# Kernel optimization log

Hardware: AMD Instinct MI355X
Metric: run time of the kernel (lower is better)

## Reference

```python
import jax, jax.numpy as jnp
import numpy as np

HIDDEN = 4096
N_HEADS = 32
N_KV_HEADS = 8
HEAD_DIM = 128
ROPE_THETA = 10000.0


def setup_inputs() -> dict:
    key = jax.random.key(0)
    ks = jax.random.split(key, 5)
    B, S = 1, 2048
    scale = 0.02
    return {
        "hidden_states": jax.random.normal(ks[0], (B, S, HIDDEN), dtype=jnp.float32),
        "q_w": jax.random.normal(ks[1], (N_HEADS * HEAD_DIM, HIDDEN), dtype=jnp.float32) * scale,
        "k_w": jax.random.normal(ks[2], (N_KV_HEADS * HEAD_DIM, HIDDEN), dtype=jnp.float32) * scale,
        "v_w": jax.random.normal(ks[3], (N_KV_HEADS * HEAD_DIM, HIDDEN), dtype=jnp.float32) * scale,
        "o_w": jax.random.normal(ks[4], (HIDDEN, N_HEADS * HEAD_DIM), dtype=jnp.float32) * scale,
        "position_ids": jnp.arange(S, dtype=jnp.int64 if jax.config.jax_enable_x64 else jnp.int32)[None, :],
    }


def _rotate_half(x):
    h = x.shape[-1] // 2
    return jnp.concatenate((-x[..., h:], x[..., :h]), axis=-1)


def _rope_cos_sin(position_ids, dtype):
    # default rope: inv_freq = theta^(-arange(0,hd,2)/hd), attention_scaling = 1
    inv_freq = 1.0 / (ROPE_THETA ** (jnp.arange(0, HEAD_DIM, 2, dtype=jnp.float32) / HEAD_DIM))
    freqs = position_ids.astype(jnp.float32)[:, :, None] * inv_freq[None, None, :]  # [B,S,hd/2]
    emb = jnp.concatenate((freqs, freqs), axis=-1)  # [B,S,hd]
    return jnp.cos(emb).astype(dtype), jnp.sin(emb).astype(dtype)


def reference(hidden_states, q_w, k_w, v_w, o_w, position_ids):
    B, S, _ = hidden_states.shape
    n_rep = N_HEADS // N_KV_HEADS

    q = (hidden_states @ q_w.T).reshape(B, S, N_HEADS, HEAD_DIM).transpose(0, 2, 1, 3)
    k = (hidden_states @ k_w.T).reshape(B, S, N_KV_HEADS, HEAD_DIM).transpose(0, 2, 1, 3)
    v = (hidden_states @ v_w.T).reshape(B, S, N_KV_HEADS, HEAD_DIM).transpose(0, 2, 1, 3)

    cos, sin = _rope_cos_sin(position_ids, hidden_states.dtype)
    cos = cos[:, None, :, :]  # unsqueeze head dim
    sin = sin[:, None, :, :]
    q = q * cos + _rotate_half(q) * sin
    k = k * cos + _rotate_half(k) * sin

    # repeat_kv (GQA)
    k = jnp.repeat(k, n_rep, axis=1)  # [B,H,S,hd]
    v = jnp.repeat(v, n_rep, axis=1)

    scale = HEAD_DIM ** -0.5
    scores = jnp.einsum("bhqd,bhkd->bhqk", q, k) * scale  # [B,H,S,S]
    causal = jnp.tril(jnp.ones((S, S), dtype=bool))
    scores = jnp.where(causal[None, None, :, :], scores, jnp.finfo(scores.dtype).min)
    probs = jax.nn.softmax(scores, axis=-1)
    attn = jnp.einsum("bhqk,bhkd->bhqd", probs, v)  # [B,H,S,hd]

    attn = attn.transpose(0, 2, 1, 3).reshape(B, S, N_HEADS * HEAD_DIM)
    return attn @ o_w.T
```

## Files before the change

kernel.cpp:

```cpp
#include <hip/hip_runtime.h>
#include <hip/hip_bf16.h>

#define NH   32
#define NKV  8
#define HD   128
#define SL   2048
#define HID  4096
#define KVW  1024
#define QKVN 6144

typedef __attribute__((ext_vector_type(8))) short short8;
typedef __attribute__((ext_vector_type(4))) float f32x4;

static __device__ __forceinline__ unsigned short f2bf(float f){
  union { float f; unsigned int i; } v; v.f = f;
  unsigned int r = v.i + 0x7FFFu + ((v.i >> 16) & 1u);
  return (unsigned short)(r >> 16);
}
static __device__ __forceinline__ float bf2f(unsigned short u){
  union { unsigned int i; float f; } v; v.i = ((unsigned int)u) << 16; return v.f;
}
static __device__ __forceinline__ unsigned int pack2(float lo, float hi){
  return (unsigned int)f2bf(lo) | ((unsigned int)f2bf(hi) << 16);
}

static __device__ __forceinline__ void gload_lds16(const void* g, void* l){
  __builtin_amdgcn_global_load_lds(
      (const __attribute__((address_space(1))) void*)g,
      (__attribute__((address_space(3))) void*)l,
      16, 0, 0);
}

__global__ void cast_f32_bf16(const float* __restrict__ src, uint4* __restrict__ dst, int n8){
  int stride = gridDim.x * blockDim.x;
  for (int i = blockIdx.x * blockDim.x + threadIdx.x; i < n8; i += stride){
    float4 a = ((const float4*)src)[2*i + 0];
    float4 b = ((const float4*)src)[2*i + 1];
    uint4 o;
    o.x = pack2(a.x, a.y); o.y = pack2(a.z, a.w);
    o.z = pack2(b.x, b.y); o.w = pack2(b.z, b.w);
    dst[i] = o;
  }
}

__global__ void rope_table_kernel(const int* __restrict__ pos, float2* __restrict__ tab){
  int i = blockIdx.x * blockDim.x + threadIdx.x;
  if (i >= SL * 64) return;
  int s = i >> 6, f = i & 63;
  float inv = expf(-((float)(2 * f) / 128.0f) * 9.210340371976184f);
  float ang = (float)pos[s] * inv;
  float sn, cs;
  sincosf(ang, &sn, &cs);
  tab[i] = make_float2(cs, sn);
}

__global__ void rope_apply_kernel(unsigned short* x, const float2* __restrict__ tab,
                                  int nheads, int rowstride){
  int i = blockIdx.x * blockDim.x + threadIdx.x;
  int total = SL * nheads * 64;
  if (i >= total) return;
  int f = i & 63;
  int t = i >> 6;
  int h = t % nheads;
  int s = t / nheads;
  float2 cs = tab[s * 64 + f];
  size_t base = (size_t)s * rowstride + h * HD;
  float x1 = bf2f(x[base + f]);
  float x2 = bf2f(x[base + f + 64]);
  x[base + f]      = f2bf(x1 * cs.x - x2 * cs.y);
  x[base + f + 64] = f2bf(x2 * cs.x + x1 * cs.y);
}

template<bool F32OUT>
__global__ __launch_bounds__(256) void gemm_bt(
  const unsigned short* __restrict__ A,
  const unsigned short* __restrict__ B,
  void* __restrict__ Cp, int M, int N, int K)
{
  __shared__ __align__(16) unsigned short As[2][128 * 32];
  __shared__ __align__(16) unsigned short Bs[2][128 * 32];
  const int tid = threadIdx.x;
  const int lane = tid & 63, wid = tid >> 6;
  const int g = lane >> 4, c15 = lane & 15;
  const int wr = wid >> 1, wc = wid & 1;

  const int gx = gridDim.x, gy = gridDim.y;
  const int nwg = gx * gy;
  const int lin = blockIdx.y * gx + blockIdx.x;
  int mb, nb;
  const int cpx = nwg >> 3;
  const int RN  = cpx >> 3;
  if (RN > 0 && (gy & 7) == 0 && (cpx & 7) == 0 && gx % RN == 0 && (8 % (gx / RN)) == 0){
    int xcd = lin & 7, j = lin >> 3;
    int nrc = gx / RN;
    int rr = xcd / nrc, rc = xcd % nrc;
    mb = rr * 8 + (j & 7);
    nb = rc * RN + (j >> 3);
  } else {
    mb = lin / gx; nb = lin % gx;
  }
  const int m0 = mb * 128, n0 = nb * 128;

  const int srow = wid * 32 + (lane >> 2);
  const int scol = (lane & 3) * 8;
  const unsigned short* Ag = &A[(size_t)(m0 + srow) * K + scol];
  const unsigned short* Bg = &B[(size_t)(n0 + srow) * K + scol];
  const size_t K16 = (size_t)16 * K;

  f32x4 acc[4][4] = {};

  gload_lds16(Ag,       &As[0][wid * 1024]);
  gload_lds16(Ag + K16, &As[0][wid * 1024 + 512]);
  gload_lds16(Bg,       &Bs[0][wid * 1024]);
  gload_lds16(Bg + K16, &Bs[0][wid * 1024 + 512]);
  __syncthreads();

  const int nk = K >> 5;
  for (int t = 0; t < nk; ++t){
    const int cur = t & 1;
    if (t + 1 < nk){
      const unsigned short* a2 = Ag + (size_t)(t + 1) * 32;
      const unsigned short* b2 = Bg + (size_t)(t + 1) * 32;
      const int nb2 = cur ^ 1;
      gload_lds16(a2,       &As[nb2][wid * 1024]);
      gload_lds16(a2 + K16, &As[nb2][wid * 1024 + 512]);
      gload_lds16(b2,       &Bs[nb2][wid * 1024]);
      gload_lds16(b2 + K16, &Bs[nb2][wid * 1024 + 512]);
    }
    short8 af[4], bfr[4];
#pragma unroll
    for (int m = 0; m < 4; ++m)
      af[m] = *(const short8*)(&As[cur][(wr * 64 + m * 16 + c15) * 32 + g * 8]);
#pragma unroll
    for (int n = 0; n < 4; ++n)
      bfr[n] = *(const short8*)(&Bs[cur][(wc * 64 + n * 16 + c15) * 32 + g * 8]);
#pragma unroll
    for (int m = 0; m < 4; ++m)
#pragma unroll
      for (int n = 0; n < 4; ++n)
        acc[m][n] = __builtin_amdgcn_mfma_f32_16x16x32_bf16(af[m], bfr[n], acc[m][n], 0, 0, 0);
    __syncthreads();
  }

#pragma unroll
  for (int m = 0; m < 4; ++m)
#pragma unroll
    for (int n = 0; n < 4; ++n){
      int row = m0 + wr * 64 + m * 16 + g * 4;
      int col = n0 + wc * 64 + n * 16 + c15;
      f32x4 v = acc[m][n];
      if (F32OUT){
        float* C = (float*)Cp;
#pragma unroll
        for (int r = 0; r < 4; ++r) C[(size_t)(row + r) * N + col] = v[r];
      } else {
        unsigned short* C = (unsigned short*)Cp;
#pragma unroll
        for (int r = 0; r < 4; ++r) C[(size_t)(row + r) * N + col] = f2bf(v[r]);
      }
    }
}

__global__ void transpose_v_kernel(const unsigned short* __restrict__ v, int vstride,
                                   unsigned short* __restrict__ vt){
  __shared__ unsigned short t[64][65];
  int h  = blockIdx.z;
  int d0 = blockIdx.y * 64;
  int s0 = blockIdx.x * 64;
  int c  = threadIdx.x & 63;
  int r0 = threadIdx.x >> 6;
#pragma unroll
  for (int r = r0; r < 64; r += 4) t[r][c] = v[(size_t)(s0 + r) * vstride + h * HD + d0 + c];
  __syncthreads();
#pragma unroll
  for (int r = r0; r < 64; r += 4) vt[(size_t)(h * HD + d0 + r) * SL + s0 + c] = t[c][r];
}

__global__ __launch_bounds__(512) void flash_attn_kernel(
  const unsigned short* __restrict__ Q,
  const unsigned short* __restrict__ Kb,
  const unsigned short* __restrict__ Vt,
  unsigned short* __restrict__ O)
{
  __shared__ __align__(16) unsigned short Ks[64 * 128];
  __shared__ __align__(16) unsigned short Vs[128 * 64];
  __shared__ __align__(16) unsigned short Ps[128 * 64];
  const int tid = threadIdx.x, lane = tid & 63, wid = tid >> 6;
  const int g = lane >> 4, c15 = lane & 15;
  const int kvh = blockIdx.x;
  const int yy = blockIdx.y;
  const int qb = (yy & 1) ? (yy >> 1) : (63 - (yy >> 1));
  const int h = kvh * 4 + (wid & 3);
  const int rg = wid >> 2;
  const int q0 = qb * 32;

  short8 aq[4];
  {
    size_t qrow = (size_t)(q0 + rg * 16 + c15) * QKVN + h * HD;
#pragma unroll
    for (int kk = 0; kk < 4; ++kk)
      aq[kk] = *(const short8*)(&Q[qrow + kk * 32 + g * 8]);
  }

  float m_i[4] = {-1e30f, -1e30f, -1e30f, -1e30f};
  float l_i[4] = {0.f, 0.f, 0.f, 0.f};
  f32x4 oacc[8];
#pragma unroll
  for (int df = 0; df < 8; ++df) oacc[df] = (f32x4){0.f, 0.f, 0.f, 0.f};

  const float scl2 = 0.08838834764831845f * 1.4426950408889634f;
  const int nt = (q0 + 31) / 64 + 1;
  for (int kt = 0; kt < nt; ++kt){
#pragma unroll
    for (int i = 0; i < 2; ++i){
      int ch = i * 512 + tid;
      { int r = ch >> 4, cob = (ch & 15) * 16;
        *(uint4*)((char*)Ks + r * 256 + (cob ^ ((r & 7) << 4))) =
          *(const uint4*)(&Kb[(size_t)(kt * 64 + r) * QKVN + kvh * HD + (cob >> 1)]); }
      { int r = ch >> 3, cob = (ch & 7) * 16;
        *(uint4*)((char*)Vs + r * 128 + (cob ^ ((r & 7) << 4))) =
          *(const uint4*)(&Vt[(size_t)(kvh * HD + r) * SL + kt * 64 + (cob >> 1)]); }
    }
    __syncthreads();

    f32x4 sc[4];
    __builtin_amdgcn_s_setprio(1);
#pragma unroll
    for (int f = 0; f < 4; ++f){
      sc[f] = (f32x4){0.f, 0.f, 0.f, 0.f};
#pragma unroll
      for (int kk = 0; kk < 4; ++kk){
        short8 bk = *(const short8*)((const char*)Ks + (f * 16 + c15) * 256 +
                                     ((kk * 64 + g * 16) ^ ((c15 & 7) << 4)));
        sc[f] = __builtin_amdgcn_mfma_f32_16x16x32_bf16(aq[kk], bk, sc[f], 0, 0, 0);
      }
    }
    __builtin_amdgcn_s_setprio(0);

    float p[4][4];
#pragma unroll
    for (int f = 0; f < 4; ++f){
      int col = kt * 64 + f * 16 + c15;
#pragma unroll
      for (int r = 0; r < 4; ++r){
        int row = q0 + rg * 16 + g * 4 + r;
        p[f][r] = (col <= row) ? sc[f][r] * scl2 : -1e30f;
      }
    }
#pragma unroll
    for (int r = 0; r < 4; ++r){
      float mx = fmaxf(fmaxf(p[0][r], p[1][r]), fmaxf(p[2][r], p[3][r]));
#pragma unroll
      for (int off = 1; off < 16; off <<= 1) mx = fmaxf(mx, __shfl_xor(mx, off, 64));
      float mnew = fmaxf(m_i[r], mx);
      float cf = exp2f(m_i[r] - mnew);
      float rs = 0.f;
#pragma unroll
      for (int f = 0; f < 4; ++f){ float e = exp2f(p[f][r] - mnew); p[f][r] = e; rs += e; }
#pragma unroll
      for (int off = 1; off < 16; off <<= 1) rs += __shfl_xor(rs, off, 64);
      l_i[r] = l_i[r] * cf + rs;
      m_i[r] = mnew;
#pragma unroll
      for (int df = 0; df < 8; ++df) oacc[df][r] *= cf;
    }

#pragma unroll
    for (int f = 0; f < 4; ++f)
#pragma unroll
      for (int r = 0; r < 4; ++r){
        int prow = wid * 16 + g * 4 + r;
        *(unsigned short*)((char*)Ps + prow * 128 +
                           ((((f * 16 + c15) * 2)) ^ ((prow & 7) << 4))) = f2bf(p[f][r]);
      }

    __builtin_amdgcn_s_setprio(1);
#pragma unroll
    for (int kk = 0; kk < 2; ++kk){
      short8 pa = *(const short8*)((const char*)Ps + (wid * 16 + c15) * 128 +
                                   ((kk * 64 + g * 16) ^ ((c15 & 7) << 4)));
#pragma unroll
      for (int df = 0; df < 8; ++df){
        short8 bv = *(const short8*)((const char*)Vs + (df * 16 + c15) * 128 +
                                     ((kk * 64 + g * 16) ^ ((c15 & 7) << 4)));
        oacc[df] = __builtin_amdgcn_mfma_f32_16x16x32_bf16(pa, bv, oacc[df], 0, 0, 0);
      }
    }
    __builtin_amdgcn_s_setprio(0);
    __syncthreads();
  }

#pragma unroll
  for (int df = 0; df < 8; ++df)
#pragma unroll
    for (int r = 0; r < 4; ++r){
      int row = q0 + rg * 16 + g * 4 + r;
      O[(size_t)row * HID + h * HD + df * 16 + c15] = f2bf(oacc[df][r] / l_i[r]);
    }
}

extern "C" void kernel_launch(void* const* d_in, const int* in_sizes, int n_in,
                              void* d_out, int out_size, void* d_ws, size_t ws_size,
                              hipStream_t stream)
{
  const float* hs  = (const float*)d_in[0];
  const float* qw  = (const float*)d_in[1];
  const float* kw  = (const float*)d_in[2];
  const float* vw  = (const float*)d_in[3];
  const float* ow  = (const float*)d_in[4];
  const int*   pos = (const int*)d_in[5];

  char* w = (char*)d_ws;
  auto alloc = [&](size_t bytes){ char* p = w; w += (bytes + 255) & ~(size_t)255; return p; };
  unsigned short* xb   = (unsigned short*)alloc((size_t)SL * HID * 2);
  unsigned short* wqkv = (unsigned short*)alloc((size_t)QKVN * HID * 2);
  unsigned short* owb  = (unsigned short*)alloc((size_t)HID * HID * 2);
  unsigned short* qkv  = (unsigned short*)alloc((size_t)SL * QKVN * 2);
  unsigned short* vt   = (unsigned short*)alloc((size_t)SL * KVW * 2);
  unsigned short* ab   = (unsigned short*)alloc((size_t)SL * HID * 2);
  float2*         tab  = (float2*)alloc((size_t)SL * 64 * sizeof(float2));

  auto cast = [&](const float* s, unsigned short* d, long n){
    int n8 = (int)(n / 8);
    int blocks = (n8 + 255) / 256; if (blocks > 2048) blocks = 2048;
    cast_f32_bf16<<<blocks, 256, 0, stream>>>(s, (uint4*)d, n8);
  };
  cast(hs, xb, (long)SL * HID);
  cast(qw, wqkv,                              (long)HID * HID);
  cast(kw, wqkv + (size_t)HID * HID,          (long)KVW * HID);
  cast(vw, wqkv + (size_t)(HID + KVW) * HID,  (long)KVW * HID);
  cast(ow, owb,                               (long)HID * HID);

  rope_table_kernel<<<(SL * 64 + 255) / 256, 256, 0, stream>>>(pos, tab);

  gemm_bt<false><<<dim3(QKVN / 128, SL / 128), 256, 0, stream>>>(xb, wqkv, qkv, SL, QKVN, HID);

  rope_apply_kernel<<<(SL * NH  * 64 + 255) / 256, 256, 0, stream>>>(qkv,        tab, NH,  QKVN);
  rope_apply_kernel<<<(SL * NKV * 64 + 255) / 256, 256, 0, stream>>>(qkv + HID,  tab, NKV, QKVN);

  transpose_v_kernel<<<dim3(SL / 64, HD / 64, NKV), 256, 0, stream>>>(qkv + HID + KVW, QKVN, vt);

  flash_attn_kernel<<<dim3(NKV, SL / 32), 512, 0, stream>>>(qkv, qkv + HID, vt, ab);

  gemm_bt<true><<<dim3(HID / 128, SL / 128), 256, 0, stream>>>(ab, owb, d_out, SL, HID, HID);
}
```

Before: 415.8 us.

## Prefetch K/V tiles into registers and keep softmax probabilities in registers

The flash attention kernel now loads the next K/V tile into registers while the current tile is computed, instead of doing a synchronous global-to-LDS copy each iteration. The QK^T MFMA operands are swapped so each lane holds one query column, which allows a single scalar max and sum per lane and a lazy rescale that only fires when the running max grows by more than 8. P is packed to bf16 with v_cvt_pk_bf16_f32 and redistributed through lane shuffles rather than an LDS round trip, which removes the Ps buffer. The kernel also sets a launch-bounds occupancy hint of 4, at the cost of higher register pressure and added shuffle work.

Result: faster. 366.5 us (-11.9%).

```diff
diff --git a/kernel.cpp b/kernel.cpp
--- a/kernel.cpp
+++ b/kernel.cpp
@@ -22,6 +22,11 @@
 }
 static __device__ __forceinline__ unsigned int pack2(float lo, float hi){
   return (unsigned int)f2bf(lo) | ((unsigned int)f2bf(hi) << 16);
+}
+static __device__ __forceinline__ unsigned int cvtpk(float lo, float hi){
+  unsigned int d;
+  asm("v_cvt_pk_bf16_f32 %0, %1, %2" : "=v"(d) : "v"(lo), "v"(hi));
+  return d;
 }
 
 static __device__ __forceinline__ void gload_lds16(const void* g, void* l){
@@ -176,7 +181,7 @@
   for (int r = r0; r < 64; r += 4) vt[(size_t)(h * HD + d0 + r) * SL + s0 + c] = t[c][r];
 }
 
-__global__ __launch_bounds__(512) void flash_attn_kernel(
+__global__ __launch_bounds__(512, 4) void flash_attn_kernel(
   const unsigned short* __restrict__ Q,
   const unsigned short* __restrict__ Kb,
   const unsigned short* __restrict__ Vt,
@@ -184,7 +189,6 @@
 {
   __shared__ __align__(16) unsigned short Ks[64 * 128];
   __shared__ __align__(16) unsigned short Vs[128 * 64];
-  __shared__ __align__(16) unsigned short Ps[128 * 64];
   const int tid = threadIdx.x, lane = tid & 63, wid = tid >> 6;
   const int g = lane >> 4, c15 = lane & 15;
   const int kvh = blockIdx.x;
@@ -193,17 +197,30 @@
   const int h = kvh * 4 + (wid & 3);
   const int rg = wid >> 2;
   const int q0 = qb * 32;
+  const int qg = q0 + rg * 16 + c15;
 
   short8 aq[4];
   {
-    size_t qrow = (size_t)(q0 + rg * 16 + c15) * QKVN + h * HD;
+    size_t qrow = (size_t)qg * QKVN + h * HD;
 #pragma unroll
     for (int kk = 0; kk < 4; ++kk)
       aq[kk] = *(const short8*)(&Q[qrow + kk * 32 + g * 8]);
   }
 
-  float m_i[4] = {-1e30f, -1e30f, -1e30f, -1e30f};
-  float l_i[4] = {0.f, 0.f, 0.f, 0.f};
+  const int krow = tid >> 3, kcol = (tid & 7) * 8;
+  const int vrow = tid >> 2, vcol = (tid & 3) * 8;
+  const unsigned short* Kgb = Kb + (size_t)kvh * HD;
+  const unsigned short* Vgb = Vt + ((size_t)kvh * HD + vrow) * SL;
+
+  uint4 kr0, kr1, vr0, vr1;
+  {
+    const unsigned short* kg = Kgb + (size_t)krow * QKVN + kcol;
+    kr0 = *(const uint4*)kg; kr1 = *(const uint4*)(kg + 64);
+    const unsigned short* vg = Vgb + vcol;
+    vr0 = *(const uint4*)vg; vr1 = *(const uint4*)(vg + 32);
+  }
+
+  float m_i = -1e30f, l_i = 0.f;
   f32x4 oacc[8];
 #pragma unroll
   for (int df = 0; df < 8; ++df) oacc[df] = (f32x4){0.f, 0.f, 0.f, 0.f};
@@ -211,17 +228,18 @@
   const float scl2 = 0.08838834764831845f * 1.4426950408889634f;
   const int nt = (q0 + 31) / 64 + 1;
   for (int kt = 0; kt < nt; ++kt){
-#pragma unroll
-    for (int i = 0; i < 2; ++i){
-      int ch = i * 512 + tid;
-      { int r = ch >> 4, cob = (ch & 15) * 16;
-        *(uint4*)((char*)Ks + r * 256 + (cob ^ ((r & 7) << 4))) =
-          *(const uint4*)(&Kb[(size_t)(kt * 64 + r) * QKVN + kvh * HD + (cob >> 1)]); }
-      { int r = ch >> 3, cob = (ch & 7) * 16;
-        *(uint4*)((char*)Vs + r * 128 + (cob ^ ((r & 7) << 4))) =
-          *(const uint4*)(&Vt[(size_t)(kvh * HD + r) * SL + kt * 64 + (cob >> 1)]); }
-    }
+    *(uint4*)((char*)Ks + krow * 256 + (( kcol * 2       ) ^ ((krow & 7) << 4))) = kr0;
+    *(uint4*)((char*)Ks + krow * 256 + (((kcol * 2) + 128) ^ ((krow & 7) << 4))) = kr1;
+    *(uint4*)((char*)Vs + vrow * 128 + (( vcol * 2       ) ^ ((vrow & 7) << 4))) = vr0;
+    *(uint4*)((char*)Vs + vrow * 128 + (((vcol * 2) +  64) ^ ((vrow & 7) << 4))) = vr1;
     __syncthreads();
+
+    if (kt + 1 < nt){
+      const unsigned short* kg = Kgb + (size_t)((kt + 1) * 64 + krow) * QKVN + kcol;
+      kr0 = *(const uint4*)kg; kr1 = *(const uint4*)(kg + 64);
+      const unsigned short* vg = Vgb + (kt + 1) * 64 + vcol;
+      vr0 = *(const uint4*)vg; vr1 = *(const uint4*)(vg + 32);
+    }
 
     f32x4 sc[4];
     __builtin_amdgcn_s_setprio(1);
@@ -232,70 +250,94 @@
       for (int kk = 0; kk < 4; ++kk){
         short8 bk = *(const short8*)((const char*)Ks + (f * 16 + c15) * 256 +
                                      ((kk * 64 + g * 16) ^ ((c15 & 7) << 4)));
-        sc[f] = __builtin_amdgcn_mfma_f32_16x16x32_bf16(aq[kk], bk, sc[f], 0, 0, 0);
+        sc[f] = __builtin_amdgcn_mfma_f32_16x16x32_bf16(bk, aq[kk], sc[f], 0, 0, 0);
       }
     }
     __builtin_amdgcn_s_setprio(0);
 
     float p[4][4];
 #pragma unroll
+    for (int f = 0; f < 4; ++f)
+#pragma unroll
+      for (int r = 0; r < 4; ++r){
+        int kvg = kt * 64 + f * 16 + g * 4 + r;
+        p[f][r] = (kvg <= qg) ? sc[f][r] * scl2 : -1e30f;
+      }
+
+    float pmax = p[0][0];
+#pragma unroll
+    for (int f = 0; f < 4; ++f)
+#pragma unroll
+      for (int r = 0; r < 4; ++r) pmax = fmaxf(pmax, p[f][r]);
+    pmax = fmaxf(pmax, __shfl_xor(pmax, 16, 64));
+    pmax = fmaxf(pmax, __shfl_xor(pmax, 32, 64));
+
+    if (!__all(pmax - m_i <= 8.0f)){
+      float mnew = fmaxf(m_i, pmax);
+      float cf = exp2f(m_i - mnew);
+      float cfr[4];
+#pragma unroll
+      for (int r = 0; r < 4; ++r) cfr[r] = __shfl(cf, (lane & 48) | (g * 4 + r), 64);
+#pragma unroll
+      for (int df = 0; df < 8; ++df)
+#pragma unroll
+        for (int r = 0; r < 4; ++r) oacc[df][r] *= cfr[r];
+      l_i *= cf;
+      m_i = mnew;
+    }
+
+    float lsum = 0.f;
+#pragma unroll
+    for (int f = 0; f < 4; ++f)
+#pragma unroll
+      for (int r = 0; r < 4; ++r){ float e = exp2f(p[f][r] - m_i); p[f][r] = e; lsum += e; }
+    lsum += __shfl_xor(lsum, 16, 64);
+    lsum += __shfl_xor(lsum, 32, 64);
+    l_i += lsum;
+
+    unsigned int pd[4][2];
+#pragma unroll
     for (int f = 0; f < 4; ++f){
-      int col = kt * 64 + f * 16 + c15;
-#pragma unroll
-      for (int r = 0; r < 4; ++r){
-        int row = q0 + rg * 16 + g * 4 + r;
-        p[f][r] = (col <= row) ? sc[f][r] * scl2 : -1e30f;
-      }
-    }
-#pragma unroll
-    for (int r = 0; r < 4; ++r){
-      float mx = fmaxf(fmaxf(p[0][r], p[1][r]), fmaxf(p[2][r], p[3][r]));
-#pragma unroll
-      for (int off = 1; off < 16; off <<= 1) mx = fmaxf(mx, __shfl_xor(mx, off, 64));
-      float mnew = fmaxf(m_i[r], mx);
-      float cf = exp2f(m_i[r] - mnew);
-      float rs = 0.f;
-#pragma unroll
-      for (int f = 0; f < 4; ++f){ float e = exp2f(p[f][r] - mnew); p[f][r] = e; rs += e; }
-#pragma unroll
-      for (int off = 1; off < 16; off <<= 1) rs += __shfl_xor(rs, off, 64);
-      l_i[r] = l_i[r] * cf + rs;
-      m_i[r] = mnew;
-#pragma unroll
-      for (int df = 0; df < 8; ++df) oacc[df][r] *= cf;
-    }
-
-#pragma unroll
-    for (int f = 0; f < 4; ++f)
-#pragma unroll
-      for (int r = 0; r < 4; ++r){
-        int prow = wid * 16 + g * 4 + r;
-        *(unsigned short*)((char*)Ps + prow * 128 +
-                           ((((f * 16 + c15) * 2)) ^ ((prow & 7) << 4))) = f2bf(p[f][r]);
-      }
-
-    __builtin_amdgcn_s_setprio(1);
+      pd[f][0] = cvtpk(p[f][0], p[f][1]);
+      pd[f][1] = cvtpk(p[f][2], p[f][3]);
+    }
+
+    const int src0 = ((g & 1) << 5) | c15;
+    const int src1 = src0 + 16;
+    const bool hiF = (g >= 2);
 #pragma unroll
     for (int kk = 0; kk < 2; ++kk){
-      short8 pa = *(const short8*)((const char*)Ps + (wid * 16 + c15) * 128 +
-                                   ((kk * 64 + g * 16) ^ ((c15 & 7) << 4)));
+      union { unsigned int u[4]; short8 s8; } pa;
+#pragma unroll
+      for (int pr = 0; pr < 2; ++pr){
+        unsigned int a0 = __shfl((int)pd[2 * kk + 0][pr], src0, 64);
+        unsigned int b0 = __shfl((int)pd[2 * kk + 1][pr], src0, 64);
+        unsigned int a1 = __shfl((int)pd[2 * kk + 0][pr], src1, 64);
+        unsigned int b1 = __shfl((int)pd[2 * kk + 1][pr], src1, 64);
+        pa.u[pr]     = hiF ? b0 : a0;
+        pa.u[2 + pr] = hiF ? b1 : a1;
+      }
+      __builtin_amdgcn_s_setprio(1);
 #pragma unroll
       for (int df = 0; df < 8; ++df){
         short8 bv = *(const short8*)((const char*)Vs + (df * 16 + c15) * 128 +
                                      ((kk * 64 + g * 16) ^ ((c15 & 7) << 4)));
-        oacc[df] = __builtin_amdgcn_mfma_f32_16x16x32_bf16(pa, bv, oacc[df], 0, 0, 0);
-      }
-    }
-    __builtin_amdgcn_s_setprio(0);
+        oacc[df] = __builtin_amdgcn_mfma_f32_16x16x32_bf16(pa.s8, bv, oacc[df], 0, 0, 0);
+      }
+      __builtin_amdgcn_s_setprio(0);
+    }
     __syncthreads();
   }
 
+  float lr[4];
+#pragma unroll
+  for (int r = 0; r < 4; ++r) lr[r] = __shfl(l_i, (lane & 48) | (g * 4 + r), 64);
 #pragma unroll
   for (int df = 0; df < 8; ++df)
 #pragma unroll
     for (int r = 0; r < 4; ++r){
       int row = q0 + rg * 16 + g * 4 + r;
-      O[(size_t)row * HID + h * HD + df * 16 + c15] = f2bf(oacc[df][r] / l_i[r]);
+      O[(size_t)row * HID + h * HD + df * 16 + c15] = f2bf(oacc[df][r] / lr[r]);
     }
 }
 
```
